# Performance work log

Hardware: AMD Instinct MI355X
Metric: run time of the kernel (lower is better)

Reference implementation:

```python
import jax, jax.numpy as jnp
import numpy as np

DELTA_BEARING = 30.0
DELTA_HEADING = 30.0
N_HEAD = int(360 / DELTA_HEADING)  # 12
N_BEAR = int(360 / DELTA_BEARING)  # 12
B, P, D = 512, 128, 64
EPS = 1e-5


def setup_inputs() -> dict:
    key = jax.random.key(0)
    ks = jax.random.split(key, 8)
    hidden_state = jax.random.normal(ks[0], (B, P, D), dtype=jnp.float32)
    distance_matrix = jax.random.uniform(ks[1], (B, P, P), dtype=jnp.float32) * 10.0
    bearing_matrix = jax.random.uniform(ks[2], (B, P, P), dtype=jnp.float32) * 360.0
    heading_matrix = jax.random.uniform(ks[3], (B, P, P), dtype=jnp.float32) * 360.0
    sequence_mask = (jax.random.uniform(ks[4], (B, P)) < 0.8).astype(jnp.float32)
    domain = jax.random.normal(ks[5], (N_HEAD, N_BEAR), dtype=jnp.float32) * 2.0 + 5.0
    W = jax.random.normal(ks[6], (D, 2 * D), dtype=jnp.float32) / np.sqrt(2 * D)
    b = jnp.zeros((D,), dtype=jnp.float32)
    return {"hidden_state": hidden_state, "distance_matrix": distance_matrix,
            "bearing_matrix": bearing_matrix, "heading_matrix": heading_matrix,
            "sequence_mask": sequence_mask, "domain": domain, "W": W, "b": b}


def reference(hidden_state, distance_matrix, bearing_matrix, heading_matrix,
              sequence_mask, domain, W, b):
    # discretized relative-pose lookup indices
    idx1 = jnp.clip(jnp.floor(heading_matrix / DELTA_HEADING), 0, N_HEAD - 1).astype(jnp.int32)
    idx2 = jnp.clip(jnp.floor(bearing_matrix / DELTA_BEARING), 0, N_BEAR - 1).astype(jnp.int32)
    # gather from learned domain table, subtract distance, relu  -> [B,P,P]
    w = jax.nn.relu(domain[idx1, idx2] - distance_matrix)
    # zero the diagonal (self-interaction) and invalid pedestrian pairs
    eye = jnp.eye(P, dtype=bool)
    pair_mask = sequence_mask[:, :, None] * sequence_mask[:, None, :]  # [B,P,P]
    w = jnp.where(eye[None, :, :], 0.0, w)
    w = jnp.where(pair_mask != 0, w, 0.0)
    # masked softmax over dim=2: mask = (w != 0)
    mask = (w != 0).astype(w.dtype)
    masked_exps = jnp.exp(w) * mask + EPS
    weights = masked_exps / (masked_exps.sum(axis=2, keepdims=True) + EPS)
    # aggregate neighbor hidden states and fuse
    weighted_hidden = jnp.einsum('bpq,bqd->bpd', weights, hidden_state)
    fused = jnp.concatenate([weighted_hidden, hidden_state], axis=2)  # [B,P,2D]
    out = jnp.tanh(fused @ W.T + b)
    return out
```

## Files before the change

### kernel.cpp

```cpp
#include <hip/hip_runtime.h>
#include <hip/hip_bf16.h>
#include <math.h>

#define NB 512
#define NP 128
#define ND 64
#define EPSF 1e-5f
#define SW 136

typedef __attribute__((ext_vector_type(8))) short short8;
typedef __attribute__((ext_vector_type(4))) float f32x4;

__device__ __forceinline__ short f2bf(float x) {
    __hip_bfloat16 h = __float2bfloat16(x);
    return *reinterpret_cast<short*>(&h);
}

__device__ __forceinline__ int bin30(float x) {
    float t = (float)((double)x * (1.0 / 30.0));
    int i = (int)t;
    return i < 0 ? 0 : (i > 11 ? 11 : i);
}

__device__ __forceinline__ float fast_tanh(float x) {
    float e = __expf(2.0f * x);
    return 1.0f - 2.0f * __builtin_amdgcn_rcpf(e + 1.0f);
}

__device__ __align__(16) short g_wbf[ND * 2 * ND];

__global__ __launch_bounds__(256) void prep_w(const float* __restrict__ W) {
    int idx = blockIdx.x * 256 + threadIdx.x;
    float4 v = ((const float4*)W)[idx];
    short4 s4;
    s4.x = f2bf(v.x); s4.y = f2bf(v.y); s4.z = f2bf(v.z); s4.w = f2bf(v.w);
    *(short4*)&g_wbf[idx * 4] = s4;
}

__global__ __launch_bounds__(256, 4) void spatial_attn_kernel(
    const float* __restrict__ hidden,
    const float* __restrict__ dist,
    const float* __restrict__ bear,
    const float* __restrict__ head,
    const float* __restrict__ smask,
    const float* __restrict__ domain,
    const float* __restrict__ bias,
    float* __restrict__ out)
{
    __shared__ __align__(16) short s_w[64 * SW];
    __shared__ __align__(16) short s_hT[ND * SW];
    __shared__ float s_dom[144];
    __shared__ float s_mask[NP];

    const int blk  = blockIdx.x;
    const int b    = blk >> 1;
    const int half = blk & 1;
    const int tid  = threadIdx.x;
    const int lane = tid & 63;
    const int wave = tid >> 6;
    const int quad = lane >> 4;
    const int l16  = lane & 15;

    {
        const float4* hsrc = (const float4*)(hidden + (size_t)b * NP * ND);
        #pragma unroll
        for (int i = 0; i < 8; ++i) {
            int idx = i * 256 + ((tid & 15) * 16 + (tid >> 4));
            float4 v = hsrc[idx];
            int q = idx >> 4;
            int d = (idx & 15) * 4;
            s_hT[(d + 0) * SW + q] = f2bf(v.x);
            s_hT[(d + 1) * SW + q] = f2bf(v.y);
            s_hT[(d + 2) * SW + q] = f2bf(v.z);
            s_hT[(d + 3) * SW + q] = f2bf(v.w);
        }
    }
    if (tid < 144) s_dom[tid] = domain[tid];
    if (tid < NP)  s_mask[tid] = smask[b * NP + tid];
    __syncthreads();

    const int R0L = wave * 16;
    const int P0  = half * 64 + R0L;
    const size_t rowbase = (size_t)b * NP * NP;

    const int rsel = lane >> 5;
    const int q0   = (lane & 31) * 4;
    const float4 mqv = *(const float4*)&s_mask[q0];

    #pragma unroll 2
    for (int j0 = 0; j0 < 16; j0 += 2) {
        const int p  = P0 + j0 + rsel;
        const int rl = R0L + j0 + rsel;
        const size_t ro = rowbase + (size_t)p * NP + q0;
        float4 dq = *(const float4*)&dist[ro];
        float4 bq = *(const float4*)&bear[ro];
        float4 hq = *(const float4*)&head[ro];
        const float mp = s_mask[p];

        float hv[4] = {hq.x, hq.y, hq.z, hq.w};
        float bv[4] = {bq.x, bq.y, bq.z, bq.w};
        float dv[4] = {dq.x, dq.y, dq.z, dq.w};
        float mv[4] = {mqv.x, mqv.y, mqv.z, mqv.w};
        short ex[4];
        #pragma unroll
        for (int c = 0; c < 4; ++c) {
            int i1 = bin30(hv[c]), i2 = bin30(bv[c]);
            float wv = s_dom[i1 * 12 + i2] - dv[c];
            bool on = (wv > 0.0f) && (mp != 0.0f) && (mv[c] != 0.0f) && (q0 + c != p);
            ex[c] = f2bf(on ? (__expf(wv) + EPSF) : EPSF);
        }
        short4 res; res.x = ex[0]; res.y = ex[1]; res.z = ex[2]; res.w = ex[3];
        *(short4*)&s_w[rl * SW + q0] = res;
    }

    f32x4 acc[4], accs;
    #pragma unroll
    for (int tj = 0; tj < 4; ++tj) acc[tj] = (f32x4){0.f, 0.f, 0.f, 0.f};
    accs = (f32x4){0.f, 0.f, 0.f, 0.f};

    short8 ones;
    #pragma unroll
    for (int i = 0; i < 8; ++i) ones[i] = (short)0x3F80;

    #pragma unroll
    for (int kb = 0; kb < 4; ++kb) {
        const int ko = kb * 32 + quad * 8;
        short8 a = *(const short8*)&s_w[(R0L + l16) * SW + ko];
        accs = __builtin_amdgcn_mfma_f32_16x16x32_bf16(a, ones, accs, 0, 0, 0);
        #pragma unroll
        for (int tj = 0; tj < 4; ++tj) {
            short8 bf = *(const short8*)&s_hT[(tj * 16 + l16) * SW + ko];
            acc[tj] = __builtin_amdgcn_mfma_f32_16x16x32_bf16(a, bf, acc[tj], 0, 0, 0);
        }
    }

    float inv[4];
    #pragma unroll
    for (int r = 0; r < 4; ++r) inv[r] = 1.0f / (accs[r] + EPSF);

    #pragma unroll
    for (int tj = 0; tj < 4; ++tj)
        #pragma unroll
        for (int r = 0; r < 4; ++r) {
            int row = R0L + quad * 4 + r;
            s_w[row * SW + tj * 16 + l16] = f2bf(acc[tj][r] * inv[r]);
        }
    #pragma unroll 4
    for (int i = 0; i < 16; ++i)
        s_w[(R0L + i) * SW + 64 + lane] = s_hT[lane * SW + (P0 + i)];

    f32x4 acc2[4];
    #pragma unroll
    for (int tj = 0; tj < 4; ++tj) acc2[tj] = (f32x4){0.f, 0.f, 0.f, 0.f};

    #pragma unroll
    for (int kb = 0; kb < 4; ++kb) {
        const int ko = kb * 32 + quad * 8;
        short8 a = *(const short8*)&s_w[(R0L + l16) * SW + ko];
        #pragma unroll
        for (int tj = 0; tj < 4; ++tj) {
            short8 bf = *(const short8*)&g_wbf[(tj * 16 + l16) * (2 * ND) + ko];
            acc2[tj] = __builtin_amdgcn_mfma_f32_16x16x32_bf16(a, bf, acc2[tj], 0, 0, 0);
        }
    }

    float bvals[4];
    #pragma unroll
    for (int tj = 0; tj < 4; ++tj) bvals[tj] = bias[tj * 16 + l16];

    float* ob = out + ((size_t)b * NP + half * 64) * ND;
    #pragma unroll
    for (int tj = 0; tj < 4; ++tj)
        #pragma unroll
        for (int r = 0; r < 4; ++r) {
            int row = R0L + quad * 4 + r;
            ob[(size_t)row * ND + tj * 16 + l16] = fast_tanh(acc2[tj][r] + bvals[tj]);
        }
}

extern "C" void kernel_launch(void* const* d_in, const int* in_sizes, int n_in,
                              void* d_out, int out_size, void* d_ws, size_t ws_size,
                              hipStream_t stream) {
    const float* hidden = (const float*)d_in[0];
    const float* dist   = (const float*)d_in[1];
    const float* bear   = (const float*)d_in[2];
    const float* head   = (const float*)d_in[3];
    const float* smask  = (const float*)d_in[4];
    const float* domain = (const float*)d_in[5];
    const float* W      = (const float*)d_in[6];
    const float* bias   = (const float*)d_in[7];
    float* out = (float*)d_out;

    prep_w<<<dim3(8), dim3(256), 0, stream>>>(W);
    spatial_attn_kernel<<<dim3(NB * 2), dim3(256), 0, stream>>>(
        hidden, dist, bear, head, smask, domain, bias, out);
}
```

Baseline: 155.8 us.

## Split exp weight computation into separate high-occupancy kernel writing bf16 workspace

```diff
diff --git a/kernel.cpp b/kernel.cpp
--- a/kernel.cpp
+++ b/kernel.cpp
@@ -37,20 +37,63 @@
     *(short4*)&g_wbf[idx * 4] = s4;
 }
 
-__global__ __launch_bounds__(256, 4) void spatial_attn_kernel(
-    const float* __restrict__ hidden,
+__global__ __launch_bounds__(256, 8) void exp_kernel(
     const float* __restrict__ dist,
     const float* __restrict__ bear,
     const float* __restrict__ head,
     const float* __restrict__ smask,
     const float* __restrict__ domain,
+    short* __restrict__ wout)
+{
+    __shared__ float s_dom[144];
+    __shared__ float s_maskq[NP];
+    __shared__ float s_maskp[16];
+
+    const int blk = blockIdx.x;
+    const int b   = blk >> 3;
+    const int p0  = (blk & 7) * 16;
+    const int tid = threadIdx.x;
+
+    if (tid < 144) s_dom[tid] = domain[tid];
+    if (tid < NP)  s_maskq[tid] = smask[b * NP + tid];
+    if (tid < 16)  s_maskp[tid] = smask[b * NP + p0 + tid];
+    __syncthreads();
+
+    const int p_loc = tid >> 4;
+    const int q0    = (tid & 15) * 8;
+    const int p     = p0 + p_loc;
+    const size_t base = ((size_t)b * NP + p) * NP + q0;
+
+    float4 d0 = *(const float4*)&dist[base], d1 = *(const float4*)&dist[base + 4];
+    float4 b0 = *(const float4*)&bear[base], b1 = *(const float4*)&bear[base + 4];
+    float4 h0 = *(const float4*)&head[base], h1 = *(const float4*)&head[base + 4];
+    const float mp = s_maskp[p_loc];
+    float4 m0 = *(const float4*)&s_maskq[q0], m1 = *(const float4*)&s_maskq[q0 + 4];
+
+    float dv[8] = {d0.x, d0.y, d0.z, d0.w, d1.x, d1.y, d1.z, d1.w};
+    float bv[8] = {b0.x, b0.y, b0.z, b0.w, b1.x, b1.y, b1.z, b1.w};
+    float hv[8] = {h0.x, h0.y, h0.z, h0.w, h1.x, h1.y, h1.z, h1.w};
+    float mv[8] = {m0.x, m0.y, m0.z, m0.w, m1.x, m1.y, m1.z, m1.w};
+
+    short8 res;
+    #pragma unroll
+    for (int c = 0; c < 8; ++c) {
+        int i1 = bin30(hv[c]), i2 = bin30(bv[c]);
+        float wv = s_dom[i1 * 12 + i2] - dv[c];
+        bool on = (wv > 0.0f) && (mp != 0.0f) && (mv[c] != 0.0f) && (q0 + c != p);
+        res[c] = f2bf(on ? (__expf(wv) + EPSF) : EPSF);
+    }
+    *(short8*)&wout[base] = res;
+}
+
+__global__ __launch_bounds__(256, 4) void fuse_kernel(
+    const short* __restrict__ wbuf,
+    const float* __restrict__ hidden,
     const float* __restrict__ bias,
     float* __restrict__ out)
 {
     __shared__ __align__(16) short s_w[64 * SW];
     __shared__ __align__(16) short s_hT[ND * SW];
-    __shared__ float s_dom[144];
-    __shared__ float s_mask[NP];
 
     const int blk  = blockIdx.x;
     const int b    = blk >> 1;
@@ -61,6 +104,16 @@
     const int quad = lane >> 4;
     const int l16  = lane & 15;
 
+    {
+        const short8* esrc = (const short8*)(wbuf + ((size_t)b * NP + half * 64) * NP);
+        #pragma unroll
+        for (int i = 0; i < 4; ++i) {
+            int idx = tid + i * 256;
+            int row = idx >> 4;
+            int col = (idx & 15) * 8;
+            *(short8*)&s_w[row * SW + col] = esrc[idx];
+        }
+    }
     {
         const float4* hsrc = (const float4*)(hidden + (size_t)b * NP * ND);
         #pragma unroll
@@ -75,43 +128,10 @@
             s_hT[(d + 3) * SW + q] = f2bf(v.w);
         }
     }
-    if (tid < 144) s_dom[tid] = domain[tid];
-    if (tid < NP)  s_mask[tid] = smask[b * NP + tid];
     __syncthreads();
 
     const int R0L = wave * 16;
     const int P0  = half * 64 + R0L;
-    const size_t rowbase = (size_t)b * NP * NP;
-
-    const int rsel = lane >> 5;
-    const int q0   = (lane & 31) * 4;
-    const float4 mqv = *(const float4*)&s_mask[q0];
-
-    #pragma unroll 2
-    for (int j0 = 0; j0 < 16; j0 += 2) {
-        const int p  = P0 + j0 + rsel;
-        const int rl = R0L + j0 + rsel;
-        const size_t ro = rowbase + (size_t)p * NP + q0;
-        float4 dq = *(const float4*)&dist[ro];
-        float4 bq = *(const float4*)&bear[ro];
-        float4 hq = *(const float4*)&head[ro];
-        const float mp = s_mask[p];
-
-        float hv[4] = {hq.x, hq.y, hq.z, hq.w};
-        float bv[4] = {bq.x, bq.y, bq.z, bq.w};
-        float dv[4] = {dq.x, dq.y, dq.z, dq.w};
-        float mv[4] = {mqv.x, mqv.y, mqv.z, mqv.w};
-        short ex[4];
-        #pragma unroll
-        for (int c = 0; c < 4; ++c) {
-            int i1 = bin30(hv[c]), i2 = bin30(bv[c]);
-            float wv = s_dom[i1 * 12 + i2] - dv[c];
-            bool on = (wv > 0.0f) && (mp != 0.0f) && (mv[c] != 0.0f) && (q0 + c != p);
-            ex[c] = f2bf(on ? (__expf(wv) + EPSF) : EPSF);
-        }
-        short4 res; res.x = ex[0]; res.y = ex[1]; res.z = ex[2]; res.w = ex[3];
-        *(short4*)&s_w[rl * SW + q0] = res;
-    }
 
     f32x4 acc[4], accs;
     #pragma unroll
@@ -190,8 +210,11 @@
     const float* W      = (const float*)d_in[6];
     const float* bias   = (const float*)d_in[7];
     float* out = (float*)d_out;
+    short* wbuf = (short*)d_ws;
 
     prep_w<<<dim3(8), dim3(256), 0, stream>>>(W);
-    spatial_attn_kernel<<<dim3(NB * 2), dim3(256), 0, stream>>>(
-        hidden, dist, bear, head, smask, domain, bias, out);
-}
+    exp_kernel<<<dim3(NB * 8), dim3(256), 0, stream>>>(
+        dist, bear, head, smask, domain, wbuf);
+    fuse_kernel<<<dim3(NB * 2), dim3(256), 0, stream>>>(
+        wbuf, hidden, bias, out);
+}
```

After: 164.7 us. 5.7% more time.
